# Optimization experiments

Hardware: AMD Instinct MI355X
Metric: run time of the kernel (lower is better)

## Reference

```python
import jax, jax.numpy as jnp
import numpy as np


def setup_inputs() -> dict:
    key = jax.random.key(0)
    k1, k2 = jax.random.split(key)
    B, C, h, w = 8, 128, 56, 56
    query_feature = jax.random.normal(k1, (B, C, h, w), dtype=jnp.float32)
    support_feature = jax.random.normal(k2, (B, C, h, w), dtype=jnp.float32)
    return {"query_feature": query_feature, "support_feature": support_feature}


def reference(query_feature, support_feature):
    q, s = query_feature, support_feature
    B, C, h, w = support_feature.shape
    N = h * w
    # torch .view semantics == row-major reshape (NOT a transpose)
    qf = jnp.reshape(query_feature, (B, N, C))      # [B, N, C]
    sf = jnp.reshape(support_feature, (B, C, N))    # [B, C, N]
    batch_adj = jnp.einsum('bnc,bcm->bnm', qf, sf)  # [B, N, N]
    attn = jax.nn.softmax(batch_adj, axis=-1)
    query_logits = jnp.einsum('bnm,bmc->bnc', attn, qf)          # [B, N, C]
    attention_mask = jax.nn.sigmoid(jnp.sum(batch_adj, axis=-1)) # [B, N]
    query_logits = query_logits * attention_mask[..., None]
    sf2 = jnp.reshape(support_feature, (B, N, C))   # another raw view
    support_logits = sf2 * attention_mask[..., None]
    query_logits = jnp.reshape(query_logits, (B, C, h, w))
    support_logits = jnp.reshape(support_logits, (B, C, h, w))
    return (q + query_logits, s + support_logits)
```

## Files before the change

### kernel.cpp

```cpp
#include <hip/hip_runtime.h>
#include <math.h>

#define B_ 8
#define C_ 128
#define N_ 3136
#define MT 64
#define TILES 49
#define QTBIG 128
#define QTILES 25

typedef short bf16x8 __attribute__((ext_vector_type(8)));
typedef float f32x4 __attribute__((ext_vector_type(4)));

__device__ __forceinline__ unsigned short f2bf(float f) {
    union { float f; unsigned u; } x; x.f = f;
    return (unsigned short)((x.u + 0x8000u) >> 16);
}

__device__ __forceinline__ void gl_lds16(const void* g, void* l) {
    __builtin_amdgcn_global_load_lds(
        (const __attribute__((address_space(1))) unsigned int*)g,
        (__attribute__((address_space(3))) unsigned int*)l, 16, 0, 0);
}

__global__ __launch_bounds__(256) void colsum_kernel(const float* __restrict__ s,
                                                     float* __restrict__ csum) {
    int blk = blockIdx.x;
    const float* p = s + (size_t)blk * N_;
    float acc = 0.f;
    for (int i = threadIdx.x; i < N_; i += 256) acc += p[i];
#pragma unroll
    for (int off = 32; off > 0; off >>= 1) acc += __shfl_down(acc, off, 64);
    __shared__ float part[4];
    if ((threadIdx.x & 63) == 0) part[threadIdx.x >> 6] = acc;
    __syncthreads();
    if (threadIdx.x == 0) csum[blk] = part[0] + part[1] + part[2] + part[3];
}

__global__ __launch_bounds__(256) void prep_kernel(const float* __restrict__ q,
                                                   const float* __restrict__ s,
                                                   unsigned short* __restrict__ sfT,
                                                   unsigned short* __restrict__ qfT) {
    __shared__ unsigned short T[8448];
    const int tid = threadIdx.x, bid = blockIdx.x;
    const int b = bid & 7, m0 = (bid >> 3) * 64;
    const float* sb = s + (size_t)b * C_ * N_;
    const float* qb = q + (size_t)b * C_ * N_;

    unsigned short (*TA)[132] = (unsigned short (*)[132])T;
#pragma unroll
    for (int st = 0; st < 8; ++st) {
        int idx = st * 256 + tid;
        int c = idx >> 4, m4 = (idx & 15) * 4;
        float4 v = *(const float4*)&sb[(size_t)c * N_ + m0 + m4];
        TA[m4 + 0][c] = f2bf(v.x);
        TA[m4 + 1][c] = f2bf(v.y);
        TA[m4 + 2][c] = f2bf(v.z);
        TA[m4 + 3][c] = f2bf(v.w);
    }
    __syncthreads();
    {
        unsigned short* dst = sfT + (size_t)b * N_ * C_;
#pragma unroll
        for (int st = 0; st < 4; ++st) {
            int g = st * 256 + tid;
            int mr = g >> 4, p = g & 15;
            int sw = (mr & 15) ^ ((mr >> 1) & 4);
            int lch = p ^ sw;
            const unsigned short* src = &TA[mr][lch * 8];
            ushort4 a = *(const ushort4*)src;
            ushort4 bq = *(const ushort4*)(src + 4);
            uint4 w;
            w.x = a.x | ((unsigned)a.y << 16);   w.y = a.z | ((unsigned)a.w << 16);
            w.z = bq.x | ((unsigned)bq.y << 16); w.w = bq.z | ((unsigned)bq.w << 16);
            *(uint4*)&dst[(size_t)(m0 + mr) * C_ + p * 8] = w;
        }
    }
    __syncthreads();

    unsigned short (*TB)[66] = (unsigned short (*)[66])T;
#pragma unroll
    for (int st = 0; st < 8; ++st) {
        int idx = st * 256 + tid;
        int r = idx >> 5, c4 = (idx & 31) * 4;
        float4 v = *(const float4*)&qb[(size_t)(m0 + r) * C_ + c4];
        TB[c4 + 0][r] = f2bf(v.x);
        TB[c4 + 1][r] = f2bf(v.y);
        TB[c4 + 2][r] = f2bf(v.z);
        TB[c4 + 3][r] = f2bf(v.w);
    }
    __syncthreads();
    {
        unsigned short* dstb = qfT + (size_t)b * N_ * C_;
#pragma unroll
        for (int st = 0; st < 4; ++st) {
            int g = st * 256 + tid;
            int p = g >> 7, c = g & 127;
            const unsigned short* src = &TB[c][p * 8];
            ushort2 a0 = *(const ushort2*)(src);
            ushort2 a1 = *(const ushort2*)(src + 2);
            ushort2 a2 = *(const ushort2*)(src + 4);
            ushort2 a3 = *(const ushort2*)(src + 6);
            uint4 w;
            w.x = a0.x | ((unsigned)a0.y << 16); w.y = a1.x | ((unsigned)a1.y << 16);
            w.z = a2.x | ((unsigned)a2.y << 16); w.w = a3.x | ((unsigned)a3.y << 16);
            *(uint4*)&dstb[((size_t)(m0 >> 6) * 8 + p) * (C_ * 8) + c * 8] = w;
        }
    }
}

__global__ __launch_bounds__(256, 1) void fused_full_kernel(
    const float* __restrict__ q, const float* __restrict__ s,
    const float* __restrict__ csum,
    const unsigned short* __restrict__ sfT,
    const unsigned short* __restrict__ qfT,
    float* __restrict__ out0, float* __restrict__ out1) {

    __shared__ __align__(16) unsigned short Kb[2][MT * C_];
    __shared__ __align__(16) unsigned short Vb[2][MT * C_];
    __shared__ __align__(16) float Of[2][64][132];
    __shared__ float dred[2][2][64];
    __shared__ float mskd[QTBIG];
    __shared__ float cs[C_];

    const int tid = threadIdx.x;
    const int lane = tid & 63;
    const int wave = tid >> 6;
    const int l15 = lane & 15;
    const int quad = lane >> 4;
    const int rg = wave >> 1;
    const int mg = wave & 1;
    const int bid = blockIdx.x;
    const int b = bid & 7;
    const int qt = bid >> 3;
    const int n0 = qt * QTBIG;

    const float* qb = q + (size_t)b * C_ * N_;
    const unsigned short* sfTb = sfT + (size_t)b * N_ * C_;
    const unsigned short* qfTb = qfT + (size_t)b * N_ * C_;

    const int sig_base = ((l15 >> 2) << 3) + (l15 & 3);

    if (tid < C_) cs[tid] = csum[b * C_ + tid];

#pragma unroll
    for (int st = 0; st < 4; ++st) {
        int i = st * 256 + tid;
        gl_lds16(sfTb + (size_t)(i >> 4) * C_ + (i & 15) * 8,
                 &Kb[0][(st * 256 + wave * 64) * 8]);
        gl_lds16(qfTb + (size_t)i * 8,
                 &Vb[0][(st * 256 + wave * 64) * 8]);
    }
    __syncthreads();

    bf16x8 qa[4][4];
    float dotp[4];
#pragma unroll
    for (int rt = 0; rt < 4; ++rt) {
        int grow = n0 + rg * 64 + rt * 16 + l15;
        if (grow > N_ - 1) grow = N_ - 1;
        float dp = 0.f;
#pragma unroll
        for (int ks = 0; ks < 4; ++ks) {
            int c0 = ks * 32 + quad * 8;
            float4 f0 = *(const float4*)&qb[(size_t)grow * C_ + c0];
            float4 f1 = *(const float4*)&qb[(size_t)grow * C_ + c0 + 4];
            dp += f0.x * cs[c0 + 0] + f0.y * cs[c0 + 1] +
                  f0.z * cs[c0 + 2] + f0.w * cs[c0 + 3] +
                  f1.x * cs[c0 + 4] + f1.y * cs[c0 + 5] +
                  f1.z * cs[c0 + 6] + f1.w * cs[c0 + 7];
            union { unsigned short u[8]; bf16x8 v; } t;
            t.u[0] = f2bf(f0.x); t.u[1] = f2bf(f0.y);
            t.u[2] = f2bf(f0.z); t.u[3] = f2bf(f0.w);
            t.u[4] = f2bf(f1.x); t.u[5] = f2bf(f1.y);
            t.u[6] = f2bf(f1.z); t.u[7] = f2bf(f1.w);
            qa[rt][ks] = t.v;
        }
        dotp[rt] = dp;
    }
#pragma unroll
    for (int rt = 0; rt < 4; ++rt) {
        float d = dotp[rt];
        d += __shfl_xor(d, 16, 64);
        d += __shfl_xor(d, 32, 64);
        if (mg == 0 && quad == 0) mskd[rg * 64 + rt * 16 + l15] = d;
    }

    f32x4 O[4][8];
#pragma unroll
    for (int rt = 0; rt < 4; ++rt)
#pragma unroll
        for (int nt = 0; nt < 8; ++nt) O[rt][nt] = (f32x4){0.f, 0.f, 0.f, 0.f};
    float dsum[4] = {0.f, 0.f, 0.f, 0.f};

    for (int tt = 0; tt < TILES; ++tt) {
        const int cur = tt & 1;
        __syncthreads();

        if (tt + 1 < TILES) {
            const int nxt = cur ^ 1;
            const size_t m1 = (size_t)(tt + 1) * MT;
#pragma unroll
            for (int st = 0; st < 4; ++st) {
                int i = st * 256 + tid;
                gl_lds16(sfTb + (m1 + (i >> 4)) * C_ + (i & 15) * 8,
                         &Kb[nxt][(st * 256 + wave * 64) * 8]);
                gl_lds16(qfTb + (size_t)(tt + 1) * (MT * C_) + (size_t)i * 8,
                         &Vb[nxt][(st * 256 + wave * 64) * 8]);
            }
        }

        f32x4 acc[2][4];
        __builtin_amdgcn_s_setprio(1);
#pragma unroll
        for (int ct = 0; ct < 2; ++ct) {
            const int mrow = sig_base + (ct << 2);
            const int sw = (mrow & 15) ^ ((mrow >> 1) & 4);
            const int row = mg * 32 + mrow;
#pragma unroll
            for (int rt = 0; rt < 4; ++rt) acc[ct][rt] = (f32x4){0.f, 0.f, 0.f, 0.f};
#pragma unroll
            for (int ks = 0; ks < 4; ++ks) {
                int ch = (ks * 4 + quad) ^ sw;
                bf16x8 af = *(const bf16x8*)&Kb[cur][row * C_ + ch * 8];
                acc[ct][0] = __builtin_amdgcn_mfma_f32_16x16x32_bf16(af, qa[0][ks], acc[ct][0], 0, 0, 0);
                acc[ct][1] = __builtin_amdgcn_mfma_f32_16x16x32_bf16(af, qa[1][ks], acc[ct][1], 0, 0, 0);
                acc[ct][2] = __builtin_amdgcn_mfma_f32_16x16x32_bf16(af, qa[2][ks], acc[ct][2], 0, 0, 0);
                acc[ct][3] = __builtin_amdgcn_mfma_f32_16x16x32_bf16(af, qa[3][ks], acc[ct][3], 0, 0, 0);
            }
        }
        __builtin_amdgcn_s_setprio(0);

        bf16x8 pa[4];
#pragma unroll
        for (int rt = 0; rt < 4; ++rt) {
            float e0 = __expf(acc[0][rt][0]);
            float e1 = __expf(acc[0][rt][1]);
            float e2 = __expf(acc[0][rt][2]);
            float e3 = __expf(acc[0][rt][3]);
            float e4 = __expf(acc[1][rt][0]);
            float e5 = __expf(acc[1][rt][1]);
            float e6 = __expf(acc[1][rt][2]);
            float e7 = __expf(acc[1][rt][3]);
            dsum[rt] += ((e0 + e1) + (e2 + e3)) + ((e4 + e5) + (e6 + e7));
            union { unsigned short u[8]; bf16x8 v; } pk;
            pk.u[0] = f2bf(e0); pk.u[1] = f2bf(e1);
            pk.u[2] = f2bf(e2); pk.u[3] = f2bf(e3);
            pk.u[4] = f2bf(e4); pk.u[5] = f2bf(e5);
            pk.u[6] = f2bf(e6); pk.u[7] = f2bf(e7);
            pa[rt] = pk.v;
        }

        __builtin_amdgcn_s_setprio(1);
#pragma unroll
        for (int nt = 0; nt < 8; ++nt) {
            bf16x8 vf = *(const bf16x8*)&Vb[cur][((mg * 4 + quad) * C_ + nt * 16 + l15) * 8];
            O[0][nt] = __builtin_amdgcn_mfma_f32_16x16x32_bf16(pa[0], vf, O[0][nt], 0, 0, 0);
            O[1][nt] = __builtin_amdgcn_mfma_f32_16x16x32_bf16(pa[1], vf, O[1][nt], 0, 0, 0);
            O[2][nt] = __builtin_amdgcn_mfma_f32_16x16x32_bf16(pa[2], vf, O[2][nt], 0, 0, 0);
            O[3][nt] = __builtin_amdgcn_mfma_f32_16x16x32_bf16(pa[3], vf, O[3][nt], 0, 0, 0);
        }
        __builtin_amdgcn_s_setprio(0);
    }

    float dloc[4];
#pragma unroll
    for (int rt = 0; rt < 4; ++rt) {
        float d = dsum[rt];
        d += __shfl_xor(d, 16, 64);
        d += __shfl_xor(d, 32, 64);
        dloc[rt] = d;
    }
#pragma unroll
    for (int rt = 0; rt < 4; ++rt)
        if (quad == 0) dred[mg][rg][rt * 16 + l15] = dloc[rt];

    if (mg == 1) {
#pragma unroll
        for (int rt = 0; rt < 4; ++rt)
#pragma unroll
            for (int nt = 0; nt < 8; ++nt)
#pragma unroll
                for (int r = 0; r < 4; ++r)
                    Of[rg][rt * 16 + quad * 4 + r][nt * 16 + l15] = O[rt][nt][r];
    }
    __syncthreads();
    if (mg == 0) {
#pragma unroll
        for (int rt = 0; rt < 4; ++rt)
#pragma unroll
            for (int nt = 0; nt < 8; ++nt)
#pragma unroll
                for (int r = 0; r < 4; ++r)
                    Of[rg][rt * 16 + quad * 4 + r][nt * 16 + l15] += O[rt][nt][r];
    }
    __syncthreads();

    const size_t vbase = (size_t)b * N_ * C_ + (size_t)n0 * C_;
#pragma unroll
    for (int it = 0; it < 16; ++it) {
        int row = it * 8 + (tid >> 5);
        int grow = n0 + row;
        if (grow >= N_) continue;
        int c = (tid & 31) * 4;
        int rgx = row >> 6, r64 = row & 63;
        float dt = dred[0][rgx][r64] + dred[1][rgx][r64];
        float mk = 1.0f / (1.0f + __expf(-mskd[row]));
        float scl = mk / dt;
        float om = 1.0f + mk;
        float4 o4 = *(const float4*)&Of[rgx][r64][c];
        float4 q4 = *(const float4*)&q[vbase + (size_t)row * C_ + c];
        float4 s4 = *(const float4*)&s[vbase + (size_t)row * C_ + c];
        float4 r0v, r1v;
        r0v.x = q4.x + o4.x * scl;
        r0v.y = q4.y + o4.y * scl;
        r0v.z = q4.z + o4.z * scl;
        r0v.w = q4.w + o4.w * scl;
        r1v.x = s4.x * om; r1v.y = s4.y * om;
        r1v.z = s4.z * om; r1v.w = s4.w * om;
        *(float4*)&out0[vbase + (size_t)row * C_ + c] = r0v;
        *(float4*)&out1[vbase + (size_t)row * C_ + c] = r1v;
    }
}

__global__ __launch_bounds__(256, 2) void fused_kernel(const float* __restrict__ q,
                                                       const float* __restrict__ s,
                                                       const float* __restrict__ csum,
                                                       float* __restrict__ out0,
                                                       float* __restrict__ out1) {
    __shared__ float QtT[C_][68];
    __shared__ float Kt[C_ * 32];
    __shared__ float Vt[32 * C_];
    __shared__ float PT[32][68];
    __shared__ float mask_l[64];
    __shared__ float csum_l[C_];

    const int t = threadIdx.x;
    const int l = t & 63, w = t >> 6, tx = t & 15, ty = t >> 4;
    const int bid = blockIdx.x, b = bid & 7, n0 = (bid >> 3) * 64;
    const float* qb = q + (size_t)b * C_ * N_;
    const float* sb = s + (size_t)b * C_ * N_;

#pragma unroll
    for (int jj = 0; jj < 2; ++jj) {
        int c = l + 64 * jj;
#pragma unroll
        for (int i = 0; i < 16; ++i) QtT[c][w + 4 * i] = qb[(size_t)(n0 + w + 4 * i) * C_ + c];
    }
    if (t < C_) csum_l[t] = csum[b * C_ + t];
    __syncthreads();
    if (t < 64) {
        float d = 0.f;
        for (int c = 0; c < C_; ++c) d += QtT[c][t] * csum_l[c];
        mask_l[t] = 1.0f / (1.0f + __expf(-d));
    }
    float4 Oa[4], Ob[4];
#pragma unroll
    for (int i = 0; i < 4; ++i) { Oa[i] = make_float4(0,0,0,0); Ob[i] = make_float4(0,0,0,0); }
    float m_r[4], l_r[4];
#pragma unroll
    for (int i = 0; i < 4; ++i) { m_r[i] = -3.0e38f; l_r[i] = 0.f; }

    for (int mt = 0; mt < N_ / 32; ++mt) {
        const int m0 = mt * 32;
        __syncthreads();
#pragma unroll
        for (int i = 0; i < 4; ++i) {
            int s4 = (w * 4 + i) * 64 + l;
            int c = s4 >> 3, mq = (s4 & 7) * 4;
            *(float4*)&Kt[c * 32 + mq] = *(const float4*)&sb[(size_t)c * N_ + m0 + mq];
            *(float4*)&Vt[s4 * 4] = *(const float4*)&qb[(size_t)m0 * C_ + s4 * 4];
        }
        __syncthreads();
        float a[4][2];
#pragma unroll
        for (int i = 0; i < 4; ++i) a[i][0] = a[i][1] = 0.f;
#pragma unroll 4
        for (int k = 0; k < C_; ++k) {
            const float4 qv = *(const float4*)&QtT[k][4 * ty];
            const float2 kv = *(const float2*)&Kt[k * 32 + 2 * tx];
            a[0][0] = fmaf(qv.x, kv.x, a[0][0]); a[0][1] = fmaf(qv.x, kv.y, a[0][1]);
            a[1][0] = fmaf(qv.y, kv.x, a[1][0]); a[1][1] = fmaf(qv.y, kv.y, a[1][1]);
            a[2][0] = fmaf(qv.z, kv.x, a[2][0]); a[2][1] = fmaf(qv.z, kv.y, a[2][1]);
            a[3][0] = fmaf(qv.w, kv.x, a[3][0]); a[3][1] = fmaf(qv.w, kv.y, a[3][1]);
        }
#pragma unroll
        for (int i = 0; i < 4; ++i) {
            float tm = fmaxf(a[i][0], a[i][1]);
            tm = fmaxf(tm, __shfl_xor(tm, 1, 64)); tm = fmaxf(tm, __shfl_xor(tm, 2, 64));
            tm = fmaxf(tm, __shfl_xor(tm, 4, 64)); tm = fmaxf(tm, __shfl_xor(tm, 8, 64));
            float nm = fmaxf(m_r[i], tm);
            float al = __expf(m_r[i] - nm);
            m_r[i] = nm;
            float p0 = __expf(a[i][0] - nm), p1 = __expf(a[i][1] - nm);
            float ts = p0 + p1;
            ts += __shfl_xor(ts, 1, 64); ts += __shfl_xor(ts, 2, 64);
            ts += __shfl_xor(ts, 4, 64); ts += __shfl_xor(ts, 8, 64);
            l_r[i] = l_r[i] * al + ts;
            PT[2 * tx + 0][4 * ty + i] = p0;
            PT[2 * tx + 1][4 * ty + i] = p1;
            Oa[i].x *= al; Oa[i].y *= al; Oa[i].z *= al; Oa[i].w *= al;
            Ob[i].x *= al; Ob[i].y *= al; Ob[i].z *= al; Ob[i].w *= al;
        }
        __syncthreads();
#pragma unroll 2
        for (int j = 0; j < 32; ++j) {
            const float4 pv = *(const float4*)&PT[j][4 * ty];
            const float4 v0 = *(const float4*)&Vt[j * C_ + 4 * tx];
            const float4 v1 = *(const float4*)&Vt[j * C_ + 4 * tx + 64];
            Oa[0].x = fmaf(pv.x, v0.x, Oa[0].x); Oa[0].y = fmaf(pv.x, v0.y, Oa[0].y);
            Oa[0].z = fmaf(pv.x, v0.z, Oa[0].z); Oa[0].w = fmaf(pv.x, v0.w, Oa[0].w);
            Ob[0].x = fmaf(pv.x, v1.x, Ob[0].x); Ob[0].y = fmaf(pv.x, v1.y, Ob[0].y);
            Ob[0].z = fmaf(pv.x, v1.z, Ob[0].z); Ob[0].w = fmaf(pv.x, v1.w, Ob[0].w);
            Oa[1].x = fmaf(pv.y, v0.x, Oa[1].x); Oa[1].y = fmaf(pv.y, v0.y, Oa[1].y);
            Oa[1].z = fmaf(pv.y, v0.z, Oa[1].z); Oa[1].w = fmaf(pv.y, v0.w, Oa[1].w);
            Ob[1].x = fmaf(pv.y, v1.x, Ob[1].x); Ob[1].y = fmaf(pv.y, v1.y, Ob[1].y);
            Ob[1].z = fmaf(pv.y, v1.z, Ob[1].z); Ob[1].w = fmaf(pv.y, v1.w, Ob[1].w);
            Oa[2].x = fmaf(pv.z, v0.x, Oa[2].x); Oa[2].y = fmaf(pv.z, v0.y, Oa[2].y);
            Oa[2].z = fmaf(pv.z, v0.z, Oa[2].z); Oa[2].w = fmaf(pv.z, v0.w, Oa[2].w);
            Ob[2].x = fmaf(pv.z, v1.x, Ob[2].x); Ob[2].y = fmaf(pv.z, v1.y, Ob[2].y);
            Ob[2].z = fmaf(pv.z, v1.z, Ob[2].z); Ob[2].w = fmaf(pv.z, v1.w, Ob[2].w);
            Oa[3].x = fmaf(pv.w, v0.x, Oa[3].x); Oa[3].y = fmaf(pv.w, v0.y, Oa[3].y);
            Oa[3].z = fmaf(pv.w, v0.z, Oa[3].z); Oa[3].w = fmaf(pv.w, v0.w, Oa[3].w);
            Ob[3].x = fmaf(pv.w, v1.x, Ob[3].x); Ob[3].y = fmaf(pv.w, v1.y, Ob[3].y);
            Ob[3].z = fmaf(pv.w, v1.z, Ob[3].z); Ob[3].w = fmaf(pv.w, v1.w, Ob[3].w);
        }
    }
#pragma unroll
    for (int i = 0; i < 4; ++i) {
        const int r = 4 * ty + i;
        const float mk = mask_l[r];
        const float scl = mk / l_r[i];
        const float om = 1.0f + mk;
        const size_t row = (size_t)b * C_ * N_ + (size_t)(n0 + r) * C_;
#pragma unroll
        for (int h = 0; h < 2; ++h) {
            const int c = 4 * tx + 64 * h;
            const float4 ov = h ? Ob[i] : Oa[i];
            float4 qv = *(const float4*)&qb[(size_t)(n0 + r) * C_ + c];
            float4 sv = *(const float4*)&sb[(size_t)(n0 + r) * C_ + c];
            float4 o0, o1;
            o0.x = qv.x + ov.x * scl; o0.y = qv.y + ov.y * scl;
            o0.z = qv.z + ov.z * scl; o0.w = qv.w + ov.w * scl;
            o1.x = sv.x * om; o1.y = sv.y * om; o1.z = sv.z * om; o1.w = sv.w * om;
            *(float4*)&out0[row + c] = o0;
            *(float4*)&out1[row + c] = o1;
        }
    }
}

extern "C" void kernel_launch(void* const* d_in, const int* in_sizes, int n_in,
                              void* d_out, int out_size, void* d_ws, size_t ws_size,
                              hipStream_t stream) {
    const float* q = (const float*)d_in[0];
    const float* s = (const float*)d_in[1];
    float* out0 = (float*)d_out;
    float* out1 = out0 + (size_t)B_ * C_ * N_;
    float* csum = (float*)d_ws;

    const size_t elems = (size_t)B_ * N_ * C_;
    const size_t need = 4096
                      + 2 * elems * sizeof(unsigned short);

    colsum_kernel<<<B_ * C_, 256, 0, stream>>>(s, csum);
    if (ws_size >= need) {
        unsigned short* sfT = (unsigned short*)((char*)d_ws + 4096);
        unsigned short* qfT = sfT + elems;
        prep_kernel<<<B_ * TILES, 256, 0, stream>>>(q, s, sfT, qfT);
        fused_full_kernel<<<QTILES * B_, 256, 0, stream>>>(q, s, csum, sfT, qfT, out0, out1);
    } else {
        fused_kernel<<<B_ * (N_ / 64), 256, 0, stream>>>(q, s, csum, out0, out1);
    }
}
```

Baseline: 169.8 us.

## Use 512-thread fused blocks, alias LDS, and fold column sums into prep

The fused attention kernel now runs 8 waves per block instead of 4. Each wave pair handles 32 query rows instead of 64, which halves the per-wave accumulator registers and spreads the 128-row tile across more waves. The K/V double buffers and the output reduction buffer now share one aliased LDS region, with an extra barrier before reuse. The separate colsum kernel is removed: prep_kernel accumulates column sums with shuffles and atomics into a buffer zeroed by a memset, which saves a launch but adds atomics and makes the summation order nondeterministic.

```diff
diff --git a/kernel.cpp b/kernel.cpp
--- a/kernel.cpp
+++ b/kernel.cpp
@@ -40,7 +40,8 @@
 __global__ __launch_bounds__(256) void prep_kernel(const float* __restrict__ q,
                                                    const float* __restrict__ s,
                                                    unsigned short* __restrict__ sfT,
-                                                   unsigned short* __restrict__ qfT) {
+                                                   unsigned short* __restrict__ qfT,
+                                                   float* __restrict__ csum) {
     __shared__ unsigned short T[8448];
     const int tid = threadIdx.x, bid = blockIdx.x;
     const int b = bid & 7, m0 = (bid >> 3) * 64;
@@ -57,6 +58,12 @@
         TA[m4 + 1][c] = f2bf(v.y);
         TA[m4 + 2][c] = f2bf(v.z);
         TA[m4 + 3][c] = f2bf(v.w);
+        float ps = (v.x + v.y) + (v.z + v.w);
+        ps += __shfl_xor(ps, 1, 16);
+        ps += __shfl_xor(ps, 2, 16);
+        ps += __shfl_xor(ps, 4, 16);
+        ps += __shfl_xor(ps, 8, 16);
+        if ((tid & 15) == 0) atomicAdd(&csum[b * C_ + c], ps);
     }
     __syncthreads();
     {
@@ -109,26 +116,28 @@
     }
 }
 
-__global__ __launch_bounds__(256, 1) void fused_full_kernel(
+__global__ __launch_bounds__(512, 1) void fused_full_kernel(
     const float* __restrict__ q, const float* __restrict__ s,
     const float* __restrict__ csum,
     const unsigned short* __restrict__ sfT,
     const unsigned short* __restrict__ qfT,
     float* __restrict__ out0, float* __restrict__ out1) {
 
-    __shared__ __align__(16) unsigned short Kb[2][MT * C_];
-    __shared__ __align__(16) unsigned short Vb[2][MT * C_];
-    __shared__ __align__(16) float Of[2][64][132];
-    __shared__ float dred[2][2][64];
+    __shared__ __align__(16) unsigned char SM[QTBIG * 132 * 4];
+    __shared__ float dred[2][QTBIG];
     __shared__ float mskd[QTBIG];
     __shared__ float cs[C_];
+
+    unsigned short* Kb = (unsigned short*)SM;
+    unsigned short* Vb = (unsigned short*)(SM + 32768);
+    float (*Of)[132] = (float (*)[132])SM;
 
     const int tid = threadIdx.x;
     const int lane = tid & 63;
     const int wave = tid >> 6;
     const int l15 = lane & 15;
     const int quad = lane >> 4;
-    const int rg = wave >> 1;
+    const int qs = wave >> 1;
     const int mg = wave & 1;
     const int bid = blockIdx.x;
     const int b = bid & 7;
@@ -144,20 +153,20 @@
     if (tid < C_) cs[tid] = csum[b * C_ + tid];
 
 #pragma unroll
-    for (int st = 0; st < 4; ++st) {
-        int i = st * 256 + tid;
+    for (int st = 0; st < 2; ++st) {
+        int i = st * 512 + tid;
         gl_lds16(sfTb + (size_t)(i >> 4) * C_ + (i & 15) * 8,
-                 &Kb[0][(st * 256 + wave * 64) * 8]);
+                 &Kb[(st * 512 + wave * 64) * 8]);
         gl_lds16(qfTb + (size_t)i * 8,
-                 &Vb[0][(st * 256 + wave * 64) * 8]);
-    }
-    __syncthreads();
-
-    bf16x8 qa[4][4];
-    float dotp[4];
-#pragma unroll
-    for (int rt = 0; rt < 4; ++rt) {
-        int grow = n0 + rg * 64 + rt * 16 + l15;
+                 &Vb[(st * 512 + wave * 64) * 8]);
+    }
+    __syncthreads();
+
+    bf16x8 qa[2][4];
+    float dotp[2];
+#pragma unroll
+    for (int rt = 0; rt < 2; ++rt) {
+        int grow = n0 + qs * 32 + rt * 16 + l15;
         if (grow > N_ - 1) grow = N_ - 1;
         float dp = 0.f;
 #pragma unroll
@@ -179,19 +188,19 @@
         dotp[rt] = dp;
     }
 #pragma unroll
-    for (int rt = 0; rt < 4; ++rt) {
+    for (int rt = 0; rt < 2; ++rt) {
         float d = dotp[rt];
         d += __shfl_xor(d, 16, 64);
         d += __shfl_xor(d, 32, 64);
-        if (mg == 0 && quad == 0) mskd[rg * 64 + rt * 16 + l15] = d;
-    }
-
-    f32x4 O[4][8];
-#pragma unroll
-    for (int rt = 0; rt < 4; ++rt)
+        if (mg == 0 && quad == 0) mskd[qs * 32 + rt * 16 + l15] = d;
+    }
+
+    f32x4 O[2][8];
+#pragma unroll
+    for (int rt = 0; rt < 2; ++rt)
 #pragma unroll
         for (int nt = 0; nt < 8; ++nt) O[rt][nt] = (f32x4){0.f, 0.f, 0.f, 0.f};
-    float dsum[4] = {0.f, 0.f, 0.f, 0.f};
+    float dsum[2] = {0.f, 0.f};
 
     for (int tt = 0; tt < TILES; ++tt) {
         const int cur = tt & 1;
@@ -201,39 +210,37 @@
             const int nxt = cur ^ 1;
             const size_t m1 = (size_t)(tt + 1) * MT;
 #pragma unroll
-            for (int st = 0; st < 4; ++st) {
-                int i = st * 256 + tid;
+            for (int st = 0; st < 2; ++st) {
+                int i = st * 512 + tid;
                 gl_lds16(sfTb + (m1 + (i >> 4)) * C_ + (i & 15) * 8,
-                         &Kb[nxt][(st * 256 + wave * 64) * 8]);
+                         &Kb[nxt * (MT * C_) + (st * 512 + wave * 64) * 8]);
                 gl_lds16(qfTb + (size_t)(tt + 1) * (MT * C_) + (size_t)i * 8,
-                         &Vb[nxt][(st * 256 + wave * 64) * 8]);
+                         &Vb[nxt * (MT * C_) + (st * 512 + wave * 64) * 8]);
             }
         }
 
-        f32x4 acc[2][4];
+        f32x4 acc[2][2];
         __builtin_amdgcn_s_setprio(1);
 #pragma unroll
         for (int ct = 0; ct < 2; ++ct) {
             const int mrow = sig_base + (ct << 2);
             const int sw = (mrow & 15) ^ ((mrow >> 1) & 4);
             const int row = mg * 32 + mrow;
-#pragma unroll
-            for (int rt = 0; rt < 4; ++rt) acc[ct][rt] = (f32x4){0.f, 0.f, 0.f, 0.f};
+            acc[ct][0] = (f32x4){0.f, 0.f, 0.f, 0.f};
+            acc[ct][1] = (f32x4){0.f, 0.f, 0.f, 0.f};
 #pragma unroll
             for (int ks = 0; ks < 4; ++ks) {
                 int ch = (ks * 4 + quad) ^ sw;
-                bf16x8 af = *(const bf16x8*)&Kb[cur][row * C_ + ch * 8];
+                bf16x8 af = *(const bf16x8*)&Kb[cur * (MT * C_) + row * C_ + ch * 8];
                 acc[ct][0] = __builtin_amdgcn_mfma_f32_16x16x32_bf16(af, qa[0][ks], acc[ct][0], 0, 0, 0);
                 acc[ct][1] = __builtin_amdgcn_mfma_f32_16x16x32_bf16(af, qa[1][ks], acc[ct][1], 0, 0, 0);
-                acc[ct][2] = __builtin_amdgcn_mfma_f32_16x16x32_bf16(af, qa[2][ks], acc[ct][2], 0, 0, 0);
-                acc[ct][3] = __builtin_amdgcn_mfma_f32_16x16x32_bf16(af, qa[3][ks], acc[ct][3], 0, 0, 0);
             }
         }
         __builtin_amdgcn_s_setprio(0);
 
-        bf16x8 pa[4];
-#pragma unroll
-        for (int rt = 0; rt < 4; ++rt) {
+        bf16x8 pa[2];
+#pragma unroll
+        for (int rt = 0; rt < 2; ++rt) {
             float e0 = __expf(acc[0][rt][0]);
             float e1 = __expf(acc[0][rt][1]);
             float e2 = __expf(acc[0][rt][2]);
@@ -254,61 +261,56 @@
         __builtin_amdgcn_s_setprio(1);
 #pragma unroll
         for (int nt = 0; nt < 8; ++nt) {
-            bf16x8 vf = *(const bf16x8*)&Vb[cur][((mg * 4 + quad) * C_ + nt * 16 + l15) * 8];
+            bf16x8 vf = *(const bf16x8*)&Vb[cur * (MT * C_) + ((mg * 4 + quad) * C_ + nt * 16 + l15) * 8];
             O[0][nt] = __builtin_amdgcn_mfma_f32_16x16x32_bf16(pa[0], vf, O[0][nt], 0, 0, 0);
             O[1][nt] = __builtin_amdgcn_mfma_f32_16x16x32_bf16(pa[1], vf, O[1][nt], 0, 0, 0);
-            O[2][nt] = __builtin_amdgcn_mfma_f32_16x16x32_bf16(pa[2], vf, O[2][nt], 0, 0, 0);
-            O[3][nt] = __builtin_amdgcn_mfma_f32_16x16x32_bf16(pa[3], vf, O[3][nt], 0, 0, 0);
         }
         __builtin_amdgcn_s_setprio(0);
     }
 
-    float dloc[4];
-#pragma unroll
-    for (int rt = 0; rt < 4; ++rt) {
+#pragma unroll
+    for (int rt = 0; rt < 2; ++rt) {
         float d = dsum[rt];
         d += __shfl_xor(d, 16, 64);
         d += __shfl_xor(d, 32, 64);
-        dloc[rt] = d;
-    }
-#pragma unroll
-    for (int rt = 0; rt < 4; ++rt)
-        if (quad == 0) dred[mg][rg][rt * 16 + l15] = dloc[rt];
+        if (quad == 0) dred[mg][qs * 32 + rt * 16 + l15] = d;
+    }
+
+    __syncthreads();
 
     if (mg == 1) {
 #pragma unroll
-        for (int rt = 0; rt < 4; ++rt)
+        for (int rt = 0; rt < 2; ++rt)
 #pragma unroll
             for (int nt = 0; nt < 8; ++nt)
 #pragma unroll
                 for (int r = 0; r < 4; ++r)
-                    Of[rg][rt * 16 + quad * 4 + r][nt * 16 + l15] = O[rt][nt][r];
+                    Of[qs * 32 + rt * 16 + quad * 4 + r][nt * 16 + l15] = O[rt][nt][r];
     }
     __syncthreads();
     if (mg == 0) {
 #pragma unroll
-        for (int rt = 0; rt < 4; ++rt)
+        for (int rt = 0; rt < 2; ++rt)
 #pragma unroll
             for (int nt = 0; nt < 8; ++nt)
 #pragma unroll
                 for (int r = 0; r < 4; ++r)
-                    Of[rg][rt * 16 + quad * 4 + r][nt * 16 + l15] += O[rt][nt][r];
+                    Of[qs * 32 + rt * 16 + quad * 4 + r][nt * 16 + l15] += O[rt][nt][r];
     }
     __syncthreads();
 
     const size_t vbase = (size_t)b * N_ * C_ + (size_t)n0 * C_;
 #pragma unroll
-    for (int it = 0; it < 16; ++it) {
-        int row = it * 8 + (tid >> 5);
+    for (int it = 0; it < 8; ++it) {
+        int row = it * 16 + (tid >> 5);
         int grow = n0 + row;
         if (grow >= N_) continue;
         int c = (tid & 31) * 4;
-        int rgx = row >> 6, r64 = row & 63;
-        float dt = dred[0][rgx][r64] + dred[1][rgx][r64];
+        float dt = dred[0][row] + dred[1][row];
         float mk = 1.0f / (1.0f + __expf(-mskd[row]));
         float scl = mk / dt;
         float om = 1.0f + mk;
-        float4 o4 = *(const float4*)&Of[rgx][r64][c];
+        float4 o4 = *(const float4*)&Of[row][c];
         float4 q4 = *(const float4*)&q[vbase + (size_t)row * C_ + c];
         float4 s4 = *(const float4*)&s[vbase + (size_t)row * C_ + c];
         float4 r0v, r1v;
@@ -462,13 +464,14 @@
     const size_t need = 4096
                       + 2 * elems * sizeof(unsigned short);
 
-    colsum_kernel<<<B_ * C_, 256, 0, stream>>>(s, csum);
     if (ws_size >= need) {
         unsigned short* sfT = (unsigned short*)((char*)d_ws + 4096);
         unsigned short* qfT = sfT + elems;
-        prep_kernel<<<B_ * TILES, 256, 0, stream>>>(q, s, sfT, qfT);
-        fused_full_kernel<<<QTILES * B_, 256, 0, stream>>>(q, s, csum, sfT, qfT, out0, out1);
+        hipMemsetAsync(csum, 0, B_ * C_ * sizeof(float), stream);
+        prep_kernel<<<B_ * TILES, 256, 0, stream>>>(q, s, sfT, qfT, csum);
+        fused_full_kernel<<<QTILES * B_, 512, 0, stream>>>(q, s, csum, sfT, qfT, out0, out1);
     } else {
+        colsum_kernel<<<B_ * C_, 256, 0, stream>>>(s, csum);
         fused_kernel<<<B_ * (N_ / 64), 256, 0, stream>>>(q, s, csum, out0, out1);
     }
 }
```

After: 162.2 us. 1.05x faster.

## Split key tiles across wave pairs and fuse column sums into prep

Applied to the files above, without the earlier changes.

The attention kernel now runs 512 threads per block. Two wave groups each process half of a 128-row key/value tile, and their partial outputs are merged through LDS at the end. The separate column-sum kernel is removed; the prep kernel instead writes per-slice partial column sums, which the main kernel reduces. Prep uses smaller 32-row slices to produce more blocks. The aim is more waves per query tile and one fewer launch, at the cost of a larger LDS footprint and a four-way serialized output reduction.

```diff
diff --git a/kernel.cpp b/kernel.cpp
--- a/kernel.cpp
+++ b/kernel.cpp
@@ -4,10 +4,12 @@
 #define B_ 8
 #define C_ 128
 #define N_ 3136
-#define MT 64
-#define TILES 49
+#define MT2 128
+#define NIT 25
+#define SLICES 98
 #define QTBIG 128
 #define QTILES 25
+#define CS_STRIDE 100
 
 typedef short bf16x8 __attribute__((ext_vector_type(8)));
 typedef float f32x4 __attribute__((ext_vector_type(4)));
@@ -40,29 +42,36 @@
 __global__ __launch_bounds__(256) void prep_kernel(const float* __restrict__ q,
                                                    const float* __restrict__ s,
                                                    unsigned short* __restrict__ sfT,
-                                                   unsigned short* __restrict__ qfT) {
-    __shared__ unsigned short T[8448];
+                                                   unsigned short* __restrict__ qfT,
+                                                   float* __restrict__ csump) {
+    __shared__ unsigned short T[4608];
     const int tid = threadIdx.x, bid = blockIdx.x;
-    const int b = bid & 7, m0 = (bid >> 3) * 64;
+    const int b = bid & 7, m0 = (bid >> 3) * 32;
+    const int slice = bid >> 3;
     const float* sb = s + (size_t)b * C_ * N_;
     const float* qb = q + (size_t)b * C_ * N_;
 
     unsigned short (*TA)[132] = (unsigned short (*)[132])T;
 #pragma unroll
-    for (int st = 0; st < 8; ++st) {
+    for (int st = 0; st < 4; ++st) {
         int idx = st * 256 + tid;
-        int c = idx >> 4, m4 = (idx & 15) * 4;
+        int c = idx >> 3, m4 = (idx & 7) * 4;
         float4 v = *(const float4*)&sb[(size_t)c * N_ + m0 + m4];
         TA[m4 + 0][c] = f2bf(v.x);
         TA[m4 + 1][c] = f2bf(v.y);
         TA[m4 + 2][c] = f2bf(v.z);
         TA[m4 + 3][c] = f2bf(v.w);
+        float ps = (v.x + v.y) + (v.z + v.w);
+        ps += __shfl_xor(ps, 1, 8);
+        ps += __shfl_xor(ps, 2, 8);
+        ps += __shfl_xor(ps, 4, 8);
+        if ((tid & 7) == 0) csump[((size_t)b * C_ + c) * CS_STRIDE + slice] = ps;
     }
     __syncthreads();
     {
         unsigned short* dst = sfT + (size_t)b * N_ * C_;
 #pragma unroll
-        for (int st = 0; st < 4; ++st) {
+        for (int st = 0; st < 2; ++st) {
             int g = st * 256 + tid;
             int mr = g >> 4, p = g & 15;
             int sw = (mr & 15) ^ ((mr >> 1) & 4);
@@ -78,9 +87,9 @@
     }
     __syncthreads();
 
-    unsigned short (*TB)[66] = (unsigned short (*)[66])T;
-#pragma unroll
-    for (int st = 0; st < 8; ++st) {
+    unsigned short (*TB)[34] = (unsigned short (*)[34])T;
+#pragma unroll
+    for (int st = 0; st < 4; ++st) {
         int idx = st * 256 + tid;
         int r = idx >> 5, c4 = (idx & 31) * 4;
         float4 v = *(const float4*)&qb[(size_t)(m0 + r) * C_ + c4];
@@ -92,11 +101,12 @@
     __syncthreads();
     {
         unsigned short* dstb = qfT + (size_t)b * N_ * C_;
-#pragma unroll
-        for (int st = 0; st < 4; ++st) {
+        const int tile = m0 >> 6, pbase = (m0 & 32) >> 3;
+#pragma unroll
+        for (int st = 0; st < 2; ++st) {
             int g = st * 256 + tid;
-            int p = g >> 7, c = g & 127;
-            const unsigned short* src = &TB[c][p * 8];
+            int pl = g >> 7, c = g & 127;
+            const unsigned short* src = &TB[c][pl * 8];
             ushort2 a0 = *(const ushort2*)(src);
             ushort2 a1 = *(const ushort2*)(src + 2);
             ushort2 a2 = *(const ushort2*)(src + 4);
@@ -104,31 +114,32 @@
             uint4 w;
             w.x = a0.x | ((unsigned)a0.y << 16); w.y = a1.x | ((unsigned)a1.y << 16);
             w.z = a2.x | ((unsigned)a2.y << 16); w.w = a3.x | ((unsigned)a3.y << 16);
-            *(uint4*)&dstb[((size_t)(m0 >> 6) * 8 + p) * (C_ * 8) + c * 8] = w;
-        }
-    }
-}
-
-__global__ __launch_bounds__(256, 1) void fused_full_kernel(
+            *(uint4*)&dstb[((size_t)tile * 8 + pbase + pl) * (C_ * 8) + c * 8] = w;
+        }
+    }
+}
+
+__global__ __launch_bounds__(512, 2) void fused_full_kernel(
     const float* __restrict__ q, const float* __restrict__ s,
-    const float* __restrict__ csum,
+    const float* __restrict__ csump,
     const unsigned short* __restrict__ sfT,
     const unsigned short* __restrict__ qfT,
     float* __restrict__ out0, float* __restrict__ out1) {
 
-    __shared__ __align__(16) unsigned short Kb[2][MT * C_];
-    __shared__ __align__(16) unsigned short Vb[2][MT * C_];
-    __shared__ __align__(16) float Of[2][64][132];
-    __shared__ float dred[2][2][64];
+    __shared__ __align__(16) unsigned char SM[131072];
+    __shared__ float dred[4][QTBIG];
     __shared__ float mskd[QTBIG];
     __shared__ float cs[C_];
+
+    float (*Of)[132] = (float (*)[132])SM;
 
     const int tid = threadIdx.x;
     const int lane = tid & 63;
     const int wave = tid >> 6;
     const int l15 = lane & 15;
     const int quad = lane >> 4;
-    const int rg = wave >> 1;
+    const int qs = wave >> 2;
+    const int tp = (wave >> 1) & 1;
     const int mg = wave & 1;
     const int bid = blockIdx.x;
     const int b = bid & 7;
@@ -141,15 +152,21 @@
 
     const int sig_base = ((l15 >> 2) << 3) + (l15 & 3);
 
-    if (tid < C_) cs[tid] = csum[b * C_ + tid];
-
 #pragma unroll
     for (int st = 0; st < 4; ++st) {
-        int i = st * 256 + tid;
+        int i = st * 512 + tid;
         gl_lds16(sfTb + (size_t)(i >> 4) * C_ + (i & 15) * 8,
-                 &Kb[0][(st * 256 + wave * 64) * 8]);
+                 SM + (st * 512 + wave * 64) * 16);
         gl_lds16(qfTb + (size_t)i * 8,
-                 &Vb[0][(st * 256 + wave * 64) * 8]);
+                 SM + 32768 + (st * 512 + wave * 64) * 16);
+    }
+
+    if (tid < C_) {
+        float a = 0.f;
+        const float* cp = csump + ((size_t)b * C_ + tid) * CS_STRIDE;
+#pragma unroll 7
+        for (int sl = 0; sl < SLICES; ++sl) a += cp[sl];
+        cs[tid] = a;
     }
     __syncthreads();
 
@@ -157,7 +174,7 @@
     float dotp[4];
 #pragma unroll
     for (int rt = 0; rt < 4; ++rt) {
-        int grow = n0 + rg * 64 + rt * 16 + l15;
+        int grow = n0 + qs * 64 + rt * 16 + l15;
         if (grow > N_ - 1) grow = N_ - 1;
         float dp = 0.f;
 #pragma unroll
@@ -183,7 +200,7 @@
         float d = dotp[rt];
         d += __shfl_xor(d, 16, 64);
         d += __shfl_xor(d, 32, 64);
-        if (mg == 0 && quad == 0) mskd[rg * 64 + rt * 16 + l15] = d;
+        if (tp == 0 && mg == 0 && quad == 0) mskd[qs * 64 + rt * 16 + l15] = d;
     }
 
     f32x4 O[4][8];
@@ -193,122 +210,156 @@
         for (int nt = 0; nt < 8; ++nt) O[rt][nt] = (f32x4){0.f, 0.f, 0.f, 0.f};
     float dsum[4] = {0.f, 0.f, 0.f, 0.f};
 
-    for (int tt = 0; tt < TILES; ++tt) {
-        const int cur = tt & 1;
+    for (int it = 0; it < NIT; ++it) {
+        const int cur = it & 1;
+        const int vm = (N_ - it * MT2 >= MT2) ? MT2 : (N_ - it * MT2);
         __syncthreads();
 
-        if (tt + 1 < TILES) {
+        if (it + 1 < NIT) {
             const int nxt = cur ^ 1;
-            const size_t m1 = (size_t)(tt + 1) * MT;
+            const int m1 = (it + 1) * MT2;
+            const int vmn = (N_ - m1 >= MT2) ? MT2 : (N_ - m1);
+            unsigned char* Kb = SM + nxt * 65536;
+            unsigned char* Vb = Kb + 32768;
 #pragma unroll
             for (int st = 0; st < 4; ++st) {
-                int i = st * 256 + tid;
-                gl_lds16(sfTb + (m1 + (i >> 4)) * C_ + (i & 15) * 8,
-                         &Kb[nxt][(st * 256 + wave * 64) * 8]);
-                gl_lds16(qfTb + (size_t)(tt + 1) * (MT * C_) + (size_t)i * 8,
-                         &Vb[nxt][(st * 256 + wave * 64) * 8]);
+                if (st * 32 < vmn) {
+                    int i = st * 512 + tid;
+                    gl_lds16(sfTb + ((size_t)m1 + (i >> 4)) * C_ + (i & 15) * 8,
+                             Kb + (st * 512 + wave * 64) * 16);
+                }
             }
-        }
-
-        f32x4 acc[2][4];
-        __builtin_amdgcn_s_setprio(1);
-#pragma unroll
-        for (int ct = 0; ct < 2; ++ct) {
-            const int mrow = sig_base + (ct << 2);
-            const int sw = (mrow & 15) ^ ((mrow >> 1) & 4);
-            const int row = mg * 32 + mrow;
-#pragma unroll
-            for (int rt = 0; rt < 4; ++rt) acc[ct][rt] = (f32x4){0.f, 0.f, 0.f, 0.f};
-#pragma unroll
-            for (int ks = 0; ks < 4; ++ks) {
-                int ch = (ks * 4 + quad) ^ sw;
-                bf16x8 af = *(const bf16x8*)&Kb[cur][row * C_ + ch * 8];
-                acc[ct][0] = __builtin_amdgcn_mfma_f32_16x16x32_bf16(af, qa[0][ks], acc[ct][0], 0, 0, 0);
-                acc[ct][1] = __builtin_amdgcn_mfma_f32_16x16x32_bf16(af, qa[1][ks], acc[ct][1], 0, 0, 0);
-                acc[ct][2] = __builtin_amdgcn_mfma_f32_16x16x32_bf16(af, qa[2][ks], acc[ct][2], 0, 0, 0);
-                acc[ct][3] = __builtin_amdgcn_mfma_f32_16x16x32_bf16(af, qa[3][ks], acc[ct][3], 0, 0, 0);
+#pragma unroll
+            for (int st = 0; st < 4; ++st) {
+                if (st * 32 < vmn) {
+                    int i = st * 512 + tid;
+                    gl_lds16(qfTb + (size_t)(m1 >> 6) * 8192 + (size_t)i * 8,
+                             Vb + (st * 512 + wave * 64) * 16);
+                }
             }
         }
-        __builtin_amdgcn_s_setprio(0);
-
-        bf16x8 pa[4];
-#pragma unroll
-        for (int rt = 0; rt < 4; ++rt) {
-            float e0 = __expf(acc[0][rt][0]);
-            float e1 = __expf(acc[0][rt][1]);
-            float e2 = __expf(acc[0][rt][2]);
-            float e3 = __expf(acc[0][rt][3]);
-            float e4 = __expf(acc[1][rt][0]);
-            float e5 = __expf(acc[1][rt][1]);
-            float e6 = __expf(acc[1][rt][2]);
-            float e7 = __expf(acc[1][rt][3]);
-            dsum[rt] += ((e0 + e1) + (e2 + e3)) + ((e4 + e5) + (e6 + e7));
-            union { unsigned short u[8]; bf16x8 v; } pk;
-            pk.u[0] = f2bf(e0); pk.u[1] = f2bf(e1);
-            pk.u[2] = f2bf(e2); pk.u[3] = f2bf(e3);
-            pk.u[4] = f2bf(e4); pk.u[5] = f2bf(e5);
-            pk.u[6] = f2bf(e6); pk.u[7] = f2bf(e7);
-            pa[rt] = pk.v;
-        }
-
-        __builtin_amdgcn_s_setprio(1);
-#pragma unroll
-        for (int nt = 0; nt < 8; ++nt) {
-            bf16x8 vf = *(const bf16x8*)&Vb[cur][((mg * 4 + quad) * C_ + nt * 16 + l15) * 8];
-            O[0][nt] = __builtin_amdgcn_mfma_f32_16x16x32_bf16(pa[0], vf, O[0][nt], 0, 0, 0);
-            O[1][nt] = __builtin_amdgcn_mfma_f32_16x16x32_bf16(pa[1], vf, O[1][nt], 0, 0, 0);
-            O[2][nt] = __builtin_amdgcn_mfma_f32_16x16x32_bf16(pa[2], vf, O[2][nt], 0, 0, 0);
-            O[3][nt] = __builtin_amdgcn_mfma_f32_16x16x32_bf16(pa[3], vf, O[3][nt], 0, 0, 0);
-        }
-        __builtin_amdgcn_s_setprio(0);
-    }
-
-    float dloc[4];
+
+        if (tp * 64 < vm) {
+            const unsigned short* KbS = (const unsigned short*)(SM + cur * 65536);
+            const unsigned short* VbS = (const unsigned short*)(SM + cur * 65536 + 32768) + tp * 8192;
+
+            f32x4 acc[2][4];
+            __builtin_amdgcn_s_setprio(1);
+#pragma unroll
+            for (int ct = 0; ct < 2; ++ct) {
+                const int mrow = sig_base + (ct << 2);
+                const int sw = (mrow & 15) ^ ((mrow >> 1) & 4);
+                const int row = tp * 64 + mg * 32 + mrow;
+#pragma unroll
+                for (int rt = 0; rt < 4; ++rt) acc[ct][rt] = (f32x4){0.f, 0.f, 0.f, 0.f};
+#pragma unroll
+                for (int ks = 0; ks < 4; ++ks) {
+                    int ch = (ks * 4 + quad) ^ sw;
+                    bf16x8 af = *(const bf16x8*)&KbS[row * C_ + ch * 8];
+                    acc[ct][0] = __builtin_amdgcn_mfma_f32_16x16x32_bf16(af, qa[0][ks], acc[ct][0], 0, 0, 0);
+                    acc[ct][1] = __builtin_amdgcn_mfma_f32_16x16x32_bf16(af, qa[1][ks], acc[ct][1], 0, 0, 0);
+                    acc[ct][2] = __builtin_amdgcn_mfma_f32_16x16x32_bf16(af, qa[2][ks], acc[ct][2], 0, 0, 0);
+                    acc[ct][3] = __builtin_amdgcn_mfma_f32_16x16x32_bf16(af, qa[3][ks], acc[ct][3], 0, 0, 0);
+                }
+            }
+            __builtin_amdgcn_s_setprio(0);
+
+            bf16x8 pa[4];
+#pragma unroll
+            for (int rt = 0; rt < 4; ++rt) {
+                float e0 = __expf(acc[0][rt][0]);
+                float e1 = __expf(acc[0][rt][1]);
+                float e2 = __expf(acc[0][rt][2]);
+                float e3 = __expf(acc[0][rt][3]);
+                float e4 = __expf(acc[1][rt][0]);
+                float e5 = __expf(acc[1][rt][1]);
+                float e6 = __expf(acc[1][rt][2]);
+                float e7 = __expf(acc[1][rt][3]);
+                dsum[rt] += ((e0 + e1) + (e2 + e3)) + ((e4 + e5) + (e6 + e7));
+                union { unsigned short u[8]; bf16x8 v; } pk;
+                pk.u[0] = f2bf(e0); pk.u[1] = f2bf(e1);
+                pk.u[2] = f2bf(e2); pk.u[3] = f2bf(e3);
+                pk.u[4] = f2bf(e4); pk.u[5] = f2bf(e5);
+                pk.u[6] = f2bf(e6); pk.u[7] = f2bf(e7);
+                pa[rt] = pk.v;
+            }
+
+            __builtin_amdgcn_s_setprio(1);
+#pragma unroll
+            for (int nt = 0; nt < 8; ++nt) {
+                bf16x8 vf = *(const bf16x8*)&VbS[((mg * 4 + quad) * C_ + nt * 16 + l15) * 8];
+                O[0][nt] = __builtin_amdgcn_mfma_f32_16x16x32_bf16(pa[0], vf, O[0][nt], 0, 0, 0);
+                O[1][nt] = __builtin_amdgcn_mfma_f32_16x16x32_bf16(pa[1], vf, O[1][nt], 0, 0, 0);
+                O[2][nt] = __builtin_amdgcn_mfma_f32_16x16x32_bf16(pa[2], vf, O[2][nt], 0, 0, 0);
+                O[3][nt] = __builtin_amdgcn_mfma_f32_16x16x32_bf16(pa[3], vf, O[3][nt], 0, 0, 0);
+            }
+            __builtin_amdgcn_s_setprio(0);
+        }
+    }
+
+    const int part = tp * 2 + mg;
 #pragma unroll
     for (int rt = 0; rt < 4; ++rt) {
         float d = dsum[rt];
         d += __shfl_xor(d, 16, 64);
         d += __shfl_xor(d, 32, 64);
-        dloc[rt] = d;
-    }
-#pragma unroll
-    for (int rt = 0; rt < 4; ++rt)
-        if (quad == 0) dred[mg][rg][rt * 16 + l15] = dloc[rt];
-
-    if (mg == 1) {
+        if (quad == 0) dred[part][qs * 64 + rt * 16 + l15] = d;
+    }
+    __syncthreads();
+
+    if (part == 3) {
 #pragma unroll
         for (int rt = 0; rt < 4; ++rt)
 #pragma unroll
             for (int nt = 0; nt < 8; ++nt)
 #pragma unroll
                 for (int r = 0; r < 4; ++r)
-                    Of[rg][rt * 16 + quad * 4 + r][nt * 16 + l15] = O[rt][nt][r];
-    }
-    __syncthreads();
-    if (mg == 0) {
+                    Of[qs * 64 + rt * 16 + quad * 4 + r][nt * 16 + l15] = O[rt][nt][r];
+    }
+    __syncthreads();
+    if (part == 2) {
 #pragma unroll
         for (int rt = 0; rt < 4; ++rt)
 #pragma unroll
             for (int nt = 0; nt < 8; ++nt)
 #pragma unroll
                 for (int r = 0; r < 4; ++r)
-                    Of[rg][rt * 16 + quad * 4 + r][nt * 16 + l15] += O[rt][nt][r];
+                    Of[qs * 64 + rt * 16 + quad * 4 + r][nt * 16 + l15] += O[rt][nt][r];
+    }
+    __syncthreads();
+    if (part == 1) {
+#pragma unroll
+        for (int rt = 0; rt < 4; ++rt)
+#pragma unroll
+            for (int nt = 0; nt < 8; ++nt)
+#pragma unroll
+                for (int r = 0; r < 4; ++r)
+                    Of[qs * 64 + rt * 16 + quad * 4 + r][nt * 16 + l15] += O[rt][nt][r];
+    }
+    __syncthreads();
+    if (part == 0) {
+#pragma unroll
+        for (int rt = 0; rt < 4; ++rt)
+#pragma unroll
+            for (int nt = 0; nt < 8; ++nt)
+#pragma unroll
+                for (int r = 0; r < 4; ++r)
+                    Of[qs * 64 + rt * 16 + quad * 4 + r][nt * 16 + l15] += O[rt][nt][r];
     }
     __syncthreads();
 
     const size_t vbase = (size_t)b * N_ * C_ + (size_t)n0 * C_;
 #pragma unroll
-    for (int it = 0; it < 16; ++it) {
-        int row = it * 8 + (tid >> 5);
+    for (int it2 = 0; it2 < 8; ++it2) {
+        int row = it2 * 16 + (tid >> 5);
         int grow = n0 + row;
         if (grow >= N_) continue;
         int c = (tid & 31) * 4;
-        int rgx = row >> 6, r64 = row & 63;
-        float dt = dred[0][rgx][r64] + dred[1][rgx][r64];
+        float dt = (dred[0][row] + dred[1][row]) + (dred[2][row] + dred[3][row]);
         float mk = 1.0f / (1.0f + __expf(-mskd[row]));
         float scl = mk / dt;
         float om = 1.0f + mk;
-        float4 o4 = *(const float4*)&Of[rgx][r64][c];
+        float4 o4 = *(const float4*)&Of[row][c];
         float4 q4 = *(const float4*)&q[vbase + (size_t)row * C_ + c];
         float4 s4 = *(const float4*)&s[vbase + (size_t)row * C_ + c];
         float4 r0v, r1v;
@@ -456,19 +507,21 @@
     const float* s = (const float*)d_in[1];
     float* out0 = (float*)d_out;
     float* out1 = out0 + (size_t)B_ * C_ * N_;
-    float* csum = (float*)d_ws;
 
     const size_t elems = (size_t)B_ * N_ * C_;
-    const size_t need = 4096
+    const size_t csump_sz = (size_t)B_ * C_ * CS_STRIDE;
+    const size_t need = csump_sz * sizeof(float)
                       + 2 * elems * sizeof(unsigned short);
 
-    colsum_kernel<<<B_ * C_, 256, 0, stream>>>(s, csum);
     if (ws_size >= need) {
-        unsigned short* sfT = (unsigned short*)((char*)d_ws + 4096);
+        float* csump = (float*)d_ws;
+        unsigned short* sfT = (unsigned short*)(csump + csump_sz);
         unsigned short* qfT = sfT + elems;
-        prep_kernel<<<B_ * TILES, 256, 0, stream>>>(q, s, sfT, qfT);
-        fused_full_kernel<<<QTILES * B_, 256, 0, stream>>>(q, s, csum, sfT, qfT, out0, out1);
+        prep_kernel<<<B_ * SLICES, 256, 0, stream>>>(q, s, sfT, qfT, csump);
+        fused_full_kernel<<<QTILES * B_, 512, 0, stream>>>(q, s, csump, sfT, qfT, out0, out1);
     } else {
+        float* csum = (float*)d_ws;
+        colsum_kernel<<<B_ * C_, 256, 0, stream>>>(s, csum);
         fused_kernel<<<B_ * (N_ / 64), 256, 0, stream>>>(q, s, csum, out0, out1);
     }
 }
```

Result: slower. 173.5 us (+2.2%).
